# Optimization experiments

Hardware: AMD Instinct MI355X
Metric: run time of the kernel (lower is better)

Reference implementation:

```python
import jax, jax.numpy as jnp
import numpy as np

B, NQ, N, D_IN, D_KEY, D_MODEL = 8, 2048, 2048, 512, 512, 512


def setup_inputs() -> dict:
    key = jax.random.key(0)
    k1, k2, k3, k4, k5, k6 = jax.random.split(key, 6)
    lim_k = np.sqrt(6.0 / (D_IN + D_KEY))
    lim_v = np.sqrt(6.0 / (D_IN + D_MODEL))
    return {
        "node_features": jax.random.normal(k1, (B, N, D_IN), dtype=jnp.float32),
        "query": jax.random.normal(k2, (B, NQ, D_IN), dtype=jnp.float32),
        "mask": jax.random.bernoulli(k3, 0.3, (NQ, B, N)),  # True = masked out
        "wq": jax.random.uniform(k4, (D_IN, D_KEY), jnp.float32, -lim_k, lim_k),
        "wk": jax.random.uniform(k5, (D_IN, D_KEY), jnp.float32, -lim_k, lim_k),
        "wv": jax.random.uniform(k6, (D_IN, D_MODEL), jnp.float32, -lim_v, lim_v),
    }


def reference(node_features, query, mask, wq, wk, wv):
    # Projections
    Q = query @ wq              # [B, NQ, d_key]
    K = node_features @ wk      # [B, N, d_key]
    V = node_features @ wv      # [B, N, d_model]
    # Raw scores [B, NQ, N]
    scores = jnp.einsum("bqd,bnd->bqn", Q, K)
    b, nq, n = scores.shape
    # Faithful to tf: reshape to (NQ, B, N), mask with float32.min, reshape back
    s = scores.reshape(nq, b, n)
    masked = jnp.where(mask, jnp.finfo(jnp.float32).min, s).reshape(b, nq, n)
    # Scale AFTER masking (as in the original), then softmax over keys
    attn = jax.nn.softmax(masked / jnp.sqrt(jnp.float32(K.shape[-1])), axis=-1)
    return attn @ V             # [B, NQ, d_model]
```

## Files before the change

### kernel.cpp

```cpp
#include <hip/hip_runtime.h>

typedef __attribute__((ext_vector_type(8))) short bf16x8;
typedef __attribute__((ext_vector_type(4))) float f32x4;

__device__ __forceinline__ unsigned short f2bf(float f) {
  unsigned int u = __builtin_bit_cast(unsigned int, f);
  u += 0x7fffu + ((u >> 16) & 1u);
  return (unsigned short)(u >> 16);
}

#define GLD16(gp, lp) __builtin_amdgcn_global_load_lds( \
    (const __attribute__((address_space(1))) unsigned int*)(gp), \
    (__attribute__((address_space(3))) unsigned int*)(lp), 16, 0, 0)

__global__ __launch_bounds__(256) void pack_mask(
    const unsigned char* __restrict__ m, unsigned long long* __restrict__ pm)
{
  __shared__ int mode1;
  if (threadIdx.x == 0) mode1 = 0;
  __syncthreads();

  const int g = blockIdx.x * 256 + threadIdx.x;
  const size_t base = (size_t)g * 64;

  uint4 v[4];
  const uint4* p1 = (const uint4*)(m + base);
  v[0] = p1[0]; v[1] = p1[1]; v[2] = p1[2]; v[3] = p1[3];
  unsigned int probe = 0;
#pragma unroll
  for (int j = 0; j < 4; ++j)
    probe |= (v[j].x | v[j].y | v[j].z | v[j].w);
  if (probe & 0x0000ff00u) mode1 = 1;
  __syncthreads();

  unsigned long long bits = 0;
  if (mode1) {
#pragma unroll
    for (int j = 0; j < 4; ++j) {
      unsigned int w[4] = {v[j].x, v[j].y, v[j].z, v[j].w};
#pragma unroll
      for (int q = 0; q < 4; ++q) {
        unsigned int u = w[q];
#pragma unroll
        for (int b = 0; b < 4; ++b)
          if ((u >> (8 * b)) & 0xffu) bits |= 1ull << (j * 16 + q * 4 + b);
      }
    }
  } else {
    const uint4* p4 = (const uint4*)(m + base * 4);
#pragma unroll
    for (int j = 0; j < 16; ++j) {
      uint4 w = p4[j];
      if (w.x) bits |= 1ull << (j * 4 + 0);
      if (w.y) bits |= 1ull << (j * 4 + 1);
      if (w.z) bits |= 1ull << (j * 4 + 2);
      if (w.w) bits |= 1ull << (j * 4 + 3);
    }
  }
  pm[g] = bits;
}

__global__ void prep(const float* __restrict__ query, const float* __restrict__ node,
                     const float* __restrict__ wq, const float* __restrict__ wk,
                     const float* __restrict__ wv,
                     unsigned short* __restrict__ Xq, unsigned short* __restrict__ Xn,
                     unsigned short* __restrict__ oq, unsigned short* __restrict__ ok,
                     unsigned short* __restrict__ ov, float* __restrict__ sums)
{
  const int b = blockIdx.x;
  if (b < 16384) {
    int i = b * 256 + threadIdx.x;
    const float* src;
    unsigned short* dst;
    int j;
    if (i < 2097152) { src = query; dst = Xq; j = i; }
    else             { src = node;  dst = Xn; j = i - 2097152; }
    float4 v = ((const float4*)src)[j];
    ushort4 o;
    o.x = f2bf(v.x); o.y = f2bf(v.y); o.z = f2bf(v.z); o.w = f2bf(v.w);
    ((ushort4*)dst)[j] = o;
  } else if (b < 19456) {
    int idx = (b - 16384) * 256 + threadIdx.x;
    int w = idx >> 18;
    int rem = idx & 262143;
    int n = rem >> 9, k = rem & 511;
    const float* W = (w == 0) ? wq : (w == 1) ? wk : wv;
    unsigned short* O = (w == 0) ? oq : (w == 1) ? ok : ov;
    O[n * 512 + k] = f2bf(W[k * 512 + n]);
  } else {
    int idx = (b - 19456) * 256 + threadIdx.x;
    sums[idx] = 0.0f;
  }
}

__global__ __launch_bounds__(512, 1) void gemm_scores(
    const unsigned short* __restrict__ Qg, const unsigned short* __restrict__ Kg,
    unsigned short* __restrict__ Eg, const unsigned long long* __restrict__ pm,
    float* __restrict__ sums)
{
  extern __shared__ char smem[];
  const int flat = blockIdx.x + (blockIdx.y << 3) + (blockIdx.z << 6);
  const long z = flat & 7;
  const int p = flat >> 3;
  const long bm = (long)(p & 7) * 256;
  const long bn = (long)(p >> 3) * 256;

  const unsigned short* Ab = Qg + z * 1048576;
  const unsigned short* Bb = Kg + z * 1048576;
  unsigned short* C = Eg + z * 4194304;
  const unsigned long long* pmask = pm + z * 65536;
  float* sumz = sums + z * 2048;

  const int tid = threadIdx.x;
  const int lane = tid & 63;
  const int wid = tid >> 6;
  const int wr = wid >> 1, wc = wid & 1;
  const int fr = lane & 15, fq = lane >> 4;

  const int srow = tid >> 2;
  const int sch = (tid & 3) ^ (srow & 3);

  char* bufs[4] = { smem, smem + 32768, smem + 65536, smem + 98304 };

#define STAGE_S(buf, kt) do { \
    const long k0_ = (long)(kt) << 5; \
    GLD16(Ab + (bm + srow) * 512 + k0_ + sch * 8,        (buf) + tid * 16); \
    GLD16(Ab + (bm + 128 + srow) * 512 + k0_ + sch * 8,  (buf) + 8192 + tid * 16); \
    GLD16(Bb + (bn + srow) * 512 + k0_ + sch * 8,        (buf) + 16384 + tid * 16); \
    GLD16(Bb + (bn + 128 + srow) * 512 + k0_ + sch * 8,  (buf) + 24576 + tid * 16); \
  } while (0)

  int aoff[4], boff[8];
#pragma unroll
  for (int i = 0; i < 4; ++i) {
    const int r = wr * 64 + i * 16 + fr;
    aoff[i] = r * 64 + (fq ^ (r & 3)) * 16;
  }
#pragma unroll
  for (int i = 0; i < 8; ++i) {
    const int r = wc * 128 + i * 16 + fr;
    boff[i] = 16384 + r * 64 + (fq ^ (r & 3)) * 16;
  }

  f32x4 acc[4][8] = {};

  STAGE_S(bufs[0], 0);
  STAGE_S(bufs[1], 1);
  STAGE_S(bufs[2], 2);
  char* c0 = bufs[0]; char* c1 = bufs[1]; char* c2 = bufs[2]; char* c3 = bufs[3];

  const int nk = 16;
  for (int t = 0; t < nk; ++t) {
    __builtin_amdgcn_sched_barrier(0);
    __builtin_amdgcn_s_barrier();
    if (t + 3 < nk) {
      STAGE_S(c3, t + 3);
      asm volatile("s_waitcnt vmcnt(12)" ::: "memory");
    } else if (t + 3 == nk) {
      asm volatile("s_waitcnt vmcnt(8)" ::: "memory");
    } else if (t + 2 == nk) {
      asm volatile("s_waitcnt vmcnt(4)" ::: "memory");
    } else {
      asm volatile("s_waitcnt vmcnt(0)" ::: "memory");
    }
    __builtin_amdgcn_s_barrier();
    __builtin_amdgcn_sched_barrier(0);

    bf16x8 a[4];
#pragma unroll
    for (int mi = 0; mi < 4; ++mi)
      a[mi] = *(const bf16x8*)(c0 + aoff[mi]);
    __builtin_amdgcn_s_setprio(1);
#pragma unroll
    for (int nj = 0; nj < 8; ++nj) {
      const bf16x8 b = *(const bf16x8*)(c0 + boff[nj]);
#pragma unroll
      for (int mi = 0; mi < 4; ++mi)
        acc[mi][nj] = __builtin_amdgcn_mfma_f32_16x16x32_bf16(a[mi], b, acc[mi][nj], 0, 0, 0);
    }
    __builtin_amdgcn_s_setprio(0);

    char* tmp = c0; c0 = c1; c1 = c2; c2 = c3; c3 = tmp;
  }
#undef STAGE_S

  const float SCALE = 0.04419417382415922f;
  const long wbase = (bn >> 6) + wc * 2;
#pragma unroll
  for (int mi = 0; mi < 4; ++mi) {
    const long rowb = bm + wr * 64 + mi * 16 + fq * 4;
#pragma unroll
    for (int r = 0; r < 4; ++r) {
      const long row = rowb + r;
      const unsigned long long w0 = pmask[row * 32 + wbase];
      const unsigned long long w1 = pmask[row * 32 + wbase + 1];
      unsigned short* Crow = C + row * 2048 + bn + wc * 128 + fr;
      float s = 0.f;
#pragma unroll
      for (int ni = 0; ni < 8; ++ni) {
        const unsigned long long w = (ni < 4) ? w0 : w1;
        const int sh = (ni & 3) * 16 + fr;
        float e = ((w >> sh) & 1ull) ? 0.0f : __expf(acc[mi][ni][r] * SCALE);
        s += e;
        Crow[ni * 16] = f2bf(e);
      }
      s += __shfl_xor(s, 1); s += __shfl_xor(s, 2);
      s += __shfl_xor(s, 4); s += __shfl_xor(s, 8);
      if (fr == 0) atomicAdd(&sumz[row], s);
    }
  }
}

__device__ __forceinline__ void narrow_core(
    const unsigned short* __restrict__ Ab, const unsigned short* __restrict__ Bb,
    void* __restrict__ Cb, long ldA, long ldB, long ldO, int nk,
    long bm, long bn, char* smem, int mode, const float* __restrict__ sums_ro)
{
  const int tid = threadIdx.x;
  const int lane = tid & 63;
  const int wid = tid >> 6;
  const int wr = wid >> 1, wc = wid & 1;
  const int fr = lane & 15, fq = lane >> 4;

  const int srow = tid >> 2;
  const int sch = (tid & 3) ^ (srow & 3);

  char* bufs[4] = { smem, smem + 24576, smem + 49152, smem + 73728 };

#define STAGE_N(buf, kt) do { \
    const long k0_ = (long)(kt) << 5; \
    GLD16(Ab + (bm + srow) * ldA + k0_ + sch * 8,        (buf) + tid * 16); \
    GLD16(Ab + (bm + 128 + srow) * ldA + k0_ + sch * 8,  (buf) + 8192 + tid * 16); \
    GLD16(Bb + (bn + srow) * ldB + k0_ + sch * 8,        (buf) + 16384 + tid * 16); \
  } while (0)

  int aoff[4], boff[4];
#pragma unroll
  for (int i = 0; i < 4; ++i) {
    const int ra = wr * 64 + i * 16 + fr;
    aoff[i] = ra * 64 + (fq ^ (ra & 3)) * 16;
    const int rb = wc * 64 + i * 16 + fr;
    boff[i] = 16384 + rb * 64 + (fq ^ (rb & 3)) * 16;
  }

  f32x4 acc[4][4] = {};

  STAGE_N(bufs[0], 0);
  STAGE_N(bufs[1], 1);
  STAGE_N(bufs[2], 2);
  char* c0 = bufs[0]; char* c1 = bufs[1]; char* c2 = bufs[2]; char* c3 = bufs[3];

  for (int t = 0; t < nk; ++t) {
    __builtin_amdgcn_sched_barrier(0);
    __builtin_amdgcn_s_barrier();
    if (t + 3 < nk) {
      STAGE_N(c3, t + 3);
      asm volatile("s_waitcnt vmcnt(9)" ::: "memory");
    } else if (t + 3 == nk) {
      asm volatile("s_waitcnt vmcnt(6)" ::: "memory");
    } else if (t + 2 == nk) {
      asm volatile("s_waitcnt vmcnt(3)" ::: "memory");
    } else {
      asm volatile("s_waitcnt vmcnt(0)" ::: "memory");
    }
    __builtin_amdgcn_s_barrier();
    __builtin_amdgcn_sched_barrier(0);

    bf16x8 a[4];
#pragma unroll
    for (int mi = 0; mi < 4; ++mi)
      a[mi] = *(const bf16x8*)(c0 + aoff[mi]);
    __builtin_amdgcn_s_setprio(1);
#pragma unroll
    for (int nj = 0; nj < 4; ++nj) {
      const bf16x8 b = *(const bf16x8*)(c0 + boff[nj]);
#pragma unroll
      for (int mi = 0; mi < 4; ++mi)
        acc[mi][nj] = __builtin_amdgcn_mfma_f32_16x16x32_bf16(a[mi], b, acc[mi][nj], 0, 0, 0);
    }
    __builtin_amdgcn_s_setprio(0);

    char* tmp = c0; c0 = c1; c1 = c2; c2 = c3; c3 = tmp;
  }
#undef STAGE_N

  if (mode == 0) {
    unsigned short* C = (unsigned short*)Cb;
#pragma unroll
    for (int mi = 0; mi < 4; ++mi)
#pragma unroll
      for (int nj = 0; nj < 4; ++nj) {
        const long row = bm + wr * 64 + mi * 16 + fq * 4;
        const long col = bn + wc * 64 + nj * 16 + fr;
#pragma unroll
        for (int r = 0; r < 4; ++r)
          C[(row + r) * ldO + col] = f2bf(acc[mi][nj][r]);
      }
  } else {
    float* C = (float*)Cb;
#pragma unroll
    for (int mi = 0; mi < 4; ++mi) {
      const long rowb = bm + wr * 64 + mi * 16 + fq * 4;
#pragma unroll
      for (int r = 0; r < 4; ++r) {
        const long row = rowb + r;
        const float iv = 1.0f / sums_ro[row];
        const long colb = bn + wc * 64 + fr;
#pragma unroll
        for (int nj = 0; nj < 4; ++nj)
          C[row * ldO + colb + nj * 16] = acc[mi][nj][r] * iv;
      }
    }
  }
}

__global__ __launch_bounds__(512, 1) void gemm_proj(
    const unsigned short* __restrict__ Xq, const unsigned short* __restrict__ Xn,
    const unsigned short* __restrict__ Wqt, const unsigned short* __restrict__ Wkt,
    const unsigned short* __restrict__ Wvt,
    unsigned short* __restrict__ Q, unsigned short* __restrict__ Kb,
    unsigned short* __restrict__ Vt)
{
  extern __shared__ char smem[];
  const int z = blockIdx.z;
  if (z == 0) {
    narrow_core(Xq, Wqt, Q, 512, 512, 512, 16,
                (long)blockIdx.x * 256, (long)blockIdx.y * 128, smem, 0, nullptr);
  } else if (z == 1) {
    narrow_core(Xn, Wkt, Kb, 512, 512, 512, 16,
                (long)blockIdx.x * 256, (long)blockIdx.y * 128, smem, 0, nullptr);
  } else {
    const int flat = blockIdx.x * 4 + blockIdx.y;
    narrow_core(Wvt, Xn, Vt, 512, 512, 16384, 16,
                (long)(flat >> 7) * 256, (long)(flat & 127) * 128, smem, 0, nullptr);
  }
}

__global__ __launch_bounds__(512, 1) void gemm_pv(
    const unsigned short* __restrict__ E, const unsigned short* __restrict__ Vt,
    const float* __restrict__ sums, float* __restrict__ O)
{
  extern __shared__ char smem[];
  const int flat = blockIdx.x + (blockIdx.y << 3) + (blockIdx.z << 5);
  const long z = flat & 7;
  const int p = flat >> 3;
  narrow_core(E + z * 4194304, Vt + z * 2048, O + z * 1048576,
              2048, 16384, 512, 64,
              (long)(p >> 2) * 256, (long)(p & 3) * 128, smem,
              2, sums + z * 2048);
}

extern "C" void kernel_launch(void* const* d_in, const int* in_sizes, int n_in,
                              void* d_out, int out_size, void* d_ws, size_t ws_size,
                              hipStream_t stream) {
  const float* node  = (const float*)d_in[0];
  const float* query = (const float*)d_in[1];
  const unsigned char* mask = (const unsigned char*)d_in[2];
  const float* wq = (const float*)d_in[3];
  const float* wk = (const float*)d_in[4];
  const float* wv = (const float*)d_in[5];
  float* out = (float*)d_out;

  char* ws = (char*)d_ws;
  unsigned short* Q   = (unsigned short*)(ws);
  unsigned short* Kb  = (unsigned short*)(ws + 16777216);
  unsigned short* Vt  = (unsigned short*)(ws + 33554432);
  unsigned short* E   = (unsigned short*)(ws + 50331648);
  unsigned short* Xq  = (unsigned short*)(ws + 50331648);
  unsigned short* Xn  = (unsigned short*)(ws + 50331648 + 16777216);
  unsigned short* Wqt = (unsigned short*)(ws + 50331648 + 33554432);
  unsigned short* Wkt = Wqt + 262144;
  unsigned short* Wvt = Wkt + 262144;
  float* sums = (float*)(ws + 117440512);
  unsigned long long* pm = (unsigned long long*)(ws + 118489088);

  pack_mask<<<2048, 256, 0, stream>>>(mask, pm);
  prep<<<19520, 256, 0, stream>>>(query, node, wq, wk, wv,
                                  Xq, Xn, Wqt, Wkt, Wvt, sums);

  dim3 gp(64, 4, 3);
  gemm_proj<<<gp, 512, 98304, stream>>>(Xq, Xn, Wqt, Wkt, Wvt, Q, Kb, Vt);

  dim3 gs(8, 8, 8);
  gemm_scores<<<gs, 512, 131072, stream>>>(Q, Kb, E, pm, sums);

  dim3 gv(8, 4, 8);
  gemm_pv<<<gv, 512, 98304, stream>>>(E, Vt, sums, out);
}
```

Measured before the change: 209.0 us.

## Shrink GEMM blocks to 256 threads with two blocks per CU

All three GEMM kernels move from 512-thread single-block-per-CU tiles to 256-thread blocks with launch bounds allowing two blocks per CU. The projection and PV tiles drop to 128x128, and the scores tile to 128x256 with a 3-stage pipeline in place of 4 stages. The LDS swizzle is changed to XOR with (row>>1)&3 to fit the new layout, and the grids are reindexed so the batch index varies fastest. The goal is better latency hiding through more resident waves and a better tile-to-CU balance, at the cost of less data reuse per tile and a shallower prefetch.

```diff
diff --git a/kernel.cpp b/kernel.cpp
--- a/kernel.cpp
+++ b/kernel.cpp
@@ -93,24 +93,11 @@
   }
 }
 
-__global__ __launch_bounds__(512, 1) void gemm_scores(
-    const unsigned short* __restrict__ Qg, const unsigned short* __restrict__ Kg,
-    unsigned short* __restrict__ Eg, const unsigned long long* __restrict__ pm,
-    float* __restrict__ sums)
-{
-  extern __shared__ char smem[];
-  const int flat = blockIdx.x + (blockIdx.y << 3) + (blockIdx.z << 6);
-  const long z = flat & 7;
-  const int p = flat >> 3;
-  const long bm = (long)(p & 7) * 256;
-  const long bn = (long)(p >> 3) * 256;
-
-  const unsigned short* Ab = Qg + z * 1048576;
-  const unsigned short* Bb = Kg + z * 1048576;
-  unsigned short* C = Eg + z * 4194304;
-  const unsigned long long* pmask = pm + z * 65536;
-  float* sumz = sums + z * 2048;
-
+__device__ __forceinline__ void core128(
+    const unsigned short* __restrict__ Ab, const unsigned short* __restrict__ Bb,
+    void* __restrict__ Cb, long ldA, long ldB, long ldO, int nk,
+    long bm, long bn, char* smem, int mode, const float* __restrict__ sums_ro)
+{
   const int tid = threadIdx.x;
   const int lane = tid & 63;
   const int wid = tid >> 6;
@@ -118,43 +105,39 @@
   const int fr = lane & 15, fq = lane >> 4;
 
   const int srow = tid >> 2;
-  const int sch = (tid & 3) ^ (srow & 3);
-
-  char* bufs[4] = { smem, smem + 32768, smem + 65536, smem + 98304 };
-
-#define STAGE_S(buf, kt) do { \
+  const int sch = (tid & 3) ^ ((srow >> 1) & 3);
+
+  char* bufs[4] = { smem, smem + 16384, smem + 32768, smem + 49152 };
+
+#define STAGE_C(buf, kt) do { \
     const long k0_ = (long)(kt) << 5; \
-    GLD16(Ab + (bm + srow) * 512 + k0_ + sch * 8,        (buf) + tid * 16); \
-    GLD16(Ab + (bm + 128 + srow) * 512 + k0_ + sch * 8,  (buf) + 8192 + tid * 16); \
-    GLD16(Bb + (bn + srow) * 512 + k0_ + sch * 8,        (buf) + 16384 + tid * 16); \
-    GLD16(Bb + (bn + 128 + srow) * 512 + k0_ + sch * 8,  (buf) + 24576 + tid * 16); \
+    GLD16(Ab + (bm + srow) * ldA + k0_ + sch * 8,        (buf) + tid * 16); \
+    GLD16(Ab + (bm + 64 + srow) * ldA + k0_ + sch * 8,   (buf) + 4096 + tid * 16); \
+    GLD16(Bb + (bn + srow) * ldB + k0_ + sch * 8,        (buf) + 8192 + tid * 16); \
+    GLD16(Bb + (bn + 64 + srow) * ldB + k0_ + sch * 8,   (buf) + 12288 + tid * 16); \
   } while (0)
 
-  int aoff[4], boff[8];
+  int aoff[4], boff[4];
 #pragma unroll
   for (int i = 0; i < 4; ++i) {
-    const int r = wr * 64 + i * 16 + fr;
-    aoff[i] = r * 64 + (fq ^ (r & 3)) * 16;
-  }
-#pragma unroll
-  for (int i = 0; i < 8; ++i) {
-    const int r = wc * 128 + i * 16 + fr;
-    boff[i] = 16384 + r * 64 + (fq ^ (r & 3)) * 16;
-  }
-
-  f32x4 acc[4][8] = {};
-
-  STAGE_S(bufs[0], 0);
-  STAGE_S(bufs[1], 1);
-  STAGE_S(bufs[2], 2);
+    const int ra = wr * 64 + i * 16 + fr;
+    aoff[i] = ra * 64 + (fq ^ ((ra >> 1) & 3)) * 16;
+    const int rb = wc * 64 + i * 16 + fr;
+    boff[i] = 8192 + rb * 64 + (fq ^ ((rb >> 1) & 3)) * 16;
+  }
+
+  f32x4 acc[4][4] = {};
+
+  STAGE_C(bufs[0], 0);
+  STAGE_C(bufs[1], 1);
+  STAGE_C(bufs[2], 2);
   char* c0 = bufs[0]; char* c1 = bufs[1]; char* c2 = bufs[2]; char* c3 = bufs[3];
 
-  const int nk = 16;
   for (int t = 0; t < nk; ++t) {
     __builtin_amdgcn_sched_barrier(0);
     __builtin_amdgcn_s_barrier();
     if (t + 3 < nk) {
-      STAGE_S(c3, t + 3);
+      STAGE_C(c3, t + 3);
       asm volatile("s_waitcnt vmcnt(12)" ::: "memory");
     } else if (t + 3 == nk) {
       asm volatile("s_waitcnt vmcnt(8)" ::: "memory");
@@ -172,6 +155,124 @@
       a[mi] = *(const bf16x8*)(c0 + aoff[mi]);
     __builtin_amdgcn_s_setprio(1);
 #pragma unroll
+    for (int nj = 0; nj < 4; ++nj) {
+      const bf16x8 b = *(const bf16x8*)(c0 + boff[nj]);
+#pragma unroll
+      for (int mi = 0; mi < 4; ++mi)
+        acc[mi][nj] = __builtin_amdgcn_mfma_f32_16x16x32_bf16(a[mi], b, acc[mi][nj], 0, 0, 0);
+    }
+    __builtin_amdgcn_s_setprio(0);
+
+    char* tmp = c0; c0 = c1; c1 = c2; c2 = c3; c3 = tmp;
+  }
+#undef STAGE_C
+
+  if (mode == 0) {
+    unsigned short* C = (unsigned short*)Cb;
+#pragma unroll
+    for (int mi = 0; mi < 4; ++mi)
+#pragma unroll
+      for (int nj = 0; nj < 4; ++nj) {
+        const long row = bm + wr * 64 + mi * 16 + fq * 4;
+        const long col = bn + wc * 64 + nj * 16 + fr;
+#pragma unroll
+        for (int r = 0; r < 4; ++r)
+          C[(row + r) * ldO + col] = f2bf(acc[mi][nj][r]);
+      }
+  } else {
+    float* C = (float*)Cb;
+#pragma unroll
+    for (int mi = 0; mi < 4; ++mi) {
+      const long rowb = bm + wr * 64 + mi * 16 + fq * 4;
+#pragma unroll
+      for (int r = 0; r < 4; ++r) {
+        const long row = rowb + r;
+        const float iv = 1.0f / sums_ro[row];
+        const long colb = bn + wc * 64 + fr;
+#pragma unroll
+        for (int nj = 0; nj < 4; ++nj)
+          C[row * ldO + colb + nj * 16] = acc[mi][nj][r] * iv;
+      }
+    }
+  }
+}
+
+__global__ __launch_bounds__(256, 2) void gemm_scores(
+    const unsigned short* __restrict__ Qg, const unsigned short* __restrict__ Kg,
+    unsigned short* __restrict__ Eg, const unsigned long long* __restrict__ pm,
+    float* __restrict__ sums)
+{
+  extern __shared__ char smem[];
+  const long z = blockIdx.x;
+  const long bm = (long)blockIdx.y * 128;
+  const long bn = (long)blockIdx.z * 256;
+
+  const unsigned short* Ab = Qg + z * 1048576;
+  const unsigned short* Bb = Kg + z * 1048576;
+  unsigned short* C = Eg + z * 4194304;
+  const unsigned long long* pmask = pm + z * 65536;
+  float* sumz = sums + z * 2048;
+
+  const int tid = threadIdx.x;
+  const int lane = tid & 63;
+  const int wid = tid >> 6;
+  const int wr = wid >> 1, wc = wid & 1;
+  const int fr = lane & 15, fq = lane >> 4;
+
+  const int srow = tid >> 2;
+  const int sch = (tid & 3) ^ ((srow >> 1) & 3);
+
+  char* bufs[3] = { smem, smem + 24576, smem + 49152 };
+
+#define STAGE_S(buf, kt) do { \
+    const long k0_ = (long)(kt) << 5; \
+    GLD16(Ab + (bm + srow) * 512 + k0_ + sch * 8,        (buf) + tid * 16); \
+    GLD16(Ab + (bm + 64 + srow) * 512 + k0_ + sch * 8,   (buf) + 4096 + tid * 16); \
+    GLD16(Bb + (bn + srow) * 512 + k0_ + sch * 8,        (buf) + 8192 + tid * 16); \
+    GLD16(Bb + (bn + 64 + srow) * 512 + k0_ + sch * 8,   (buf) + 12288 + tid * 16); \
+    GLD16(Bb + (bn + 128 + srow) * 512 + k0_ + sch * 8,  (buf) + 16384 + tid * 16); \
+    GLD16(Bb + (bn + 192 + srow) * 512 + k0_ + sch * 8,  (buf) + 20480 + tid * 16); \
+  } while (0)
+
+  int aoff[4], boff[8];
+#pragma unroll
+  for (int i = 0; i < 4; ++i) {
+    const int r = wr * 64 + i * 16 + fr;
+    aoff[i] = r * 64 + (fq ^ ((r >> 1) & 3)) * 16;
+  }
+#pragma unroll
+  for (int i = 0; i < 8; ++i) {
+    const int r = wc * 128 + i * 16 + fr;
+    boff[i] = 8192 + r * 64 + (fq ^ ((r >> 1) & 3)) * 16;
+  }
+
+  f32x4 acc[4][8] = {};
+
+  STAGE_S(bufs[0], 0);
+  STAGE_S(bufs[1], 1);
+  char* c0 = bufs[0]; char* c1 = bufs[1]; char* c2 = bufs[2];
+
+  const int nk = 16;
+  for (int t = 0; t < nk; ++t) {
+    __builtin_amdgcn_sched_barrier(0);
+    __builtin_amdgcn_s_barrier();
+    if (t + 2 < nk) {
+      STAGE_S(c2, t + 2);
+      asm volatile("s_waitcnt vmcnt(12)" ::: "memory");
+    } else if (t + 2 == nk) {
+      asm volatile("s_waitcnt vmcnt(6)" ::: "memory");
+    } else {
+      asm volatile("s_waitcnt vmcnt(0)" ::: "memory");
+    }
+    __builtin_amdgcn_s_barrier();
+    __builtin_amdgcn_sched_barrier(0);
+
+    bf16x8 a[4];
+#pragma unroll
+    for (int mi = 0; mi < 4; ++mi)
+      a[mi] = *(const bf16x8*)(c0 + aoff[mi]);
+    __builtin_amdgcn_s_setprio(1);
+#pragma unroll
     for (int nj = 0; nj < 8; ++nj) {
       const bf16x8 b = *(const bf16x8*)(c0 + boff[nj]);
 #pragma unroll
@@ -180,7 +281,7 @@
     }
     __builtin_amdgcn_s_setprio(0);
 
-    char* tmp = c0; c0 = c1; c1 = c2; c2 = c3; c3 = tmp;
+    char* tmp = c0; c0 = c1; c1 = c2; c2 = tmp;
   }
 #undef STAGE_S
 
@@ -211,110 +312,7 @@
   }
 }
 
-__device__ __forceinline__ void narrow_core(
-    const unsigned short* __restrict__ Ab, const unsigned short* __restrict__ Bb,
-    void* __restrict__ Cb, long ldA, long ldB, long ldO, int nk,
-    long bm, long bn, char* smem, int mode, const float* __restrict__ sums_ro)
-{
-  const int tid = threadIdx.x;
-  const int lane = tid & 63;
-  const int wid = tid >> 6;
-  const int wr = wid >> 1, wc = wid & 1;
-  const int fr = lane & 15, fq = lane >> 4;
-
-  const int srow = tid >> 2;
-  const int sch = (tid & 3) ^ (srow & 3);
-
-  char* bufs[4] = { smem, smem + 24576, smem + 49152, smem + 73728 };
-
-#define STAGE_N(buf, kt) do { \
-    const long k0_ = (long)(kt) << 5; \
-    GLD16(Ab + (bm + srow) * ldA + k0_ + sch * 8,        (buf) + tid * 16); \
-    GLD16(Ab + (bm + 128 + srow) * ldA + k0_ + sch * 8,  (buf) + 8192 + tid * 16); \
-    GLD16(Bb + (bn + srow) * ldB + k0_ + sch * 8,        (buf) + 16384 + tid * 16); \
-  } while (0)
-
-  int aoff[4], boff[4];
-#pragma unroll
-  for (int i = 0; i < 4; ++i) {
-    const int ra = wr * 64 + i * 16 + fr;
-    aoff[i] = ra * 64 + (fq ^ (ra & 3)) * 16;
-    const int rb = wc * 64 + i * 16 + fr;
-    boff[i] = 16384 + rb * 64 + (fq ^ (rb & 3)) * 16;
-  }
-
-  f32x4 acc[4][4] = {};
-
-  STAGE_N(bufs[0], 0);
-  STAGE_N(bufs[1], 1);
-  STAGE_N(bufs[2], 2);
-  char* c0 = bufs[0]; char* c1 = bufs[1]; char* c2 = bufs[2]; char* c3 = bufs[3];
-
-  for (int t = 0; t < nk; ++t) {
-    __builtin_amdgcn_sched_barrier(0);
-    __builtin_amdgcn_s_barrier();
-    if (t + 3 < nk) {
-      STAGE_N(c3, t + 3);
-      asm volatile("s_waitcnt vmcnt(9)" ::: "memory");
-    } else if (t + 3 == nk) {
-      asm volatile("s_waitcnt vmcnt(6)" ::: "memory");
-    } else if (t + 2 == nk) {
-      asm volatile("s_waitcnt vmcnt(3)" ::: "memory");
-    } else {
-      asm volatile("s_waitcnt vmcnt(0)" ::: "memory");
-    }
-    __builtin_amdgcn_s_barrier();
-    __builtin_amdgcn_sched_barrier(0);
-
-    bf16x8 a[4];
-#pragma unroll
-    for (int mi = 0; mi < 4; ++mi)
-      a[mi] = *(const bf16x8*)(c0 + aoff[mi]);
-    __builtin_amdgcn_s_setprio(1);
-#pragma unroll
-    for (int nj = 0; nj < 4; ++nj) {
-      const bf16x8 b = *(const bf16x8*)(c0 + boff[nj]);
-#pragma unroll
-      for (int mi = 0; mi < 4; ++mi)
-        acc[mi][nj] = __builtin_amdgcn_mfma_f32_16x16x32_bf16(a[mi], b, acc[mi][nj], 0, 0, 0);
-    }
-    __builtin_amdgcn_s_setprio(0);
-
-    char* tmp = c0; c0 = c1; c1 = c2; c2 = c3; c3 = tmp;
-  }
-#undef STAGE_N
-
-  if (mode == 0) {
-    unsigned short* C = (unsigned short*)Cb;
-#pragma unroll
-    for (int mi = 0; mi < 4; ++mi)
-#pragma unroll
-      for (int nj = 0; nj < 4; ++nj) {
-        const long row = bm + wr * 64 + mi * 16 + fq * 4;
-        const long col = bn + wc * 64 + nj * 16 + fr;
-#pragma unroll
-        for (int r = 0; r < 4; ++r)
-          C[(row + r) * ldO + col] = f2bf(acc[mi][nj][r]);
-      }
-  } else {
-    float* C = (float*)Cb;
-#pragma unroll
-    for (int mi = 0; mi < 4; ++mi) {
-      const long rowb = bm + wr * 64 + mi * 16 + fq * 4;
-#pragma unroll
-      for (int r = 0; r < 4; ++r) {
-        const long row = rowb + r;
-        const float iv = 1.0f / sums_ro[row];
-        const long colb = bn + wc * 64 + fr;
-#pragma unroll
-        for (int nj = 0; nj < 4; ++nj)
-          C[row * ldO + colb + nj * 16] = acc[mi][nj][r] * iv;
-      }
-    }
-  }
-}
-
-__global__ __launch_bounds__(512, 1) void gemm_proj(
+__global__ __launch_bounds__(256, 2) void gemm_proj(
     const unsigned short* __restrict__ Xq, const unsigned short* __restrict__ Xn,
     const unsigned short* __restrict__ Wqt, const unsigned short* __restrict__ Wkt,
     const unsigned short* __restrict__ Wvt,
@@ -324,30 +322,27 @@
   extern __shared__ char smem[];
   const int z = blockIdx.z;
   if (z == 0) {
-    narrow_core(Xq, Wqt, Q, 512, 512, 512, 16,
-                (long)blockIdx.x * 256, (long)blockIdx.y * 128, smem, 0, nullptr);
+    core128(Xq, Wqt, Q, 512, 512, 512, 16,
+            (long)blockIdx.x * 128, (long)blockIdx.y * 128, smem, 0, nullptr);
   } else if (z == 1) {
-    narrow_core(Xn, Wkt, Kb, 512, 512, 512, 16,
-                (long)blockIdx.x * 256, (long)blockIdx.y * 128, smem, 0, nullptr);
+    core128(Xn, Wkt, Kb, 512, 512, 512, 16,
+            (long)blockIdx.x * 128, (long)blockIdx.y * 128, smem, 0, nullptr);
   } else {
-    const int flat = blockIdx.x * 4 + blockIdx.y;
-    narrow_core(Wvt, Xn, Vt, 512, 512, 16384, 16,
-                (long)(flat >> 7) * 256, (long)(flat & 127) * 128, smem, 0, nullptr);
-  }
-}
-
-__global__ __launch_bounds__(512, 1) void gemm_pv(
+    core128(Wvt, Xn, Vt, 512, 512, 16384, 16,
+            (long)blockIdx.y * 128, (long)blockIdx.x * 128, smem, 0, nullptr);
+  }
+}
+
+__global__ __launch_bounds__(256, 2) void gemm_pv(
     const unsigned short* __restrict__ E, const unsigned short* __restrict__ Vt,
     const float* __restrict__ sums, float* __restrict__ O)
 {
   extern __shared__ char smem[];
-  const int flat = blockIdx.x + (blockIdx.y << 3) + (blockIdx.z << 5);
-  const long z = flat & 7;
-  const int p = flat >> 3;
-  narrow_core(E + z * 4194304, Vt + z * 2048, O + z * 1048576,
-              2048, 16384, 512, 64,
-              (long)(p >> 2) * 256, (long)(p & 3) * 128, smem,
-              2, sums + z * 2048);
+  const long z = blockIdx.x;
+  core128(E + z * 4194304, Vt + z * 2048, O + z * 1048576,
+          2048, 16384, 512, 64,
+          (long)blockIdx.y * 128, (long)blockIdx.z * 128, smem,
+          2, sums + z * 2048);
 }
 
 extern "C" void kernel_launch(void* const* d_in, const int* in_sizes, int n_in,
@@ -378,12 +373,12 @@
   prep<<<19520, 256, 0, stream>>>(query, node, wq, wk, wv,
                                   Xq, Xn, Wqt, Wkt, Wvt, sums);
 
-  dim3 gp(64, 4, 3);
-  gemm_proj<<<gp, 512, 98304, stream>>>(Xq, Xn, Wqt, Wkt, Wvt, Q, Kb, Vt);
-
-  dim3 gs(8, 8, 8);
-  gemm_scores<<<gs, 512, 131072, stream>>>(Q, Kb, E, pm, sums);
-
-  dim3 gv(8, 4, 8);
-  gemm_pv<<<gv, 512, 98304, stream>>>(E, Vt, sums, out);
-}
+  dim3 gp(128, 4, 3);
+  gemm_proj<<<gp, 256, 65536, stream>>>(Xq, Xn, Wqt, Wkt, Wvt, Q, Kb, Vt);
+
+  dim3 gs(8, 16, 8);
+  gemm_scores<<<gs, 256, 73728, stream>>>(Q, Kb, E, pm, sums);
+
+  dim3 gv(8, 16, 4);
+  gemm_pv<<<gv, 256, 65536, stream>>>(E, Vt, sums, out);
+}
```

Result: faster. 198.9 us (-4.8%).
